# Kernel tuning notes

Measured on AMD Instinct MI355X. Metric: run time of the kernel, lower is better.

Reference implementation:

```python
import jax, jax.numpy as jnp
import numpy as np

VOCAB, E = 50000, 256          # embedding table
WH, SH = 256, 256              # word_hidden_size, sent_hidden_size
DM = WH // 2                   # d_model of both S4Models = 128
NC = (WH // 2) // 2            # complex state modes N//2 = 64
FACTOR = 2
LN_EPS = 1e-5


def _s4model(x, encW, encb, log_dt, Cre, Cim, logAre, Aim, D,
             convW, convb, lng, lnb, d1W, d1b, d2W, d2b, pooling):
    """S4Model forward (eval mode, n_layers=1). x: (B, L, d_input)."""
    x = x @ encW + encb                      # (B, L, H)
    u = jnp.swapaxes(x, -1, -2)              # (B, H, L)
    L = u.shape[-1]
    # --- S4D kernel (Vandermonde) ---
    dt = jnp.exp(log_dt)                     # (H,)
    C = Cre + 1j * Cim                       # (H, N)
    A = -jnp.exp(logAre) + 1j * Aim          # (H, N)
    dtA = A * dt[:, None]                    # (H, N)
    K = jnp.exp(dtA[:, :, None] * jnp.arange(L))           # (H, N, L)
    Ck = C * (jnp.exp(dtA) - 1.0) / A
    k = 2.0 * jnp.einsum('hn,hnl->hl', Ck, K).real         # (H, L)
    # --- FFT convolution ---
    kf = jnp.fft.rfft(k, n=2 * L)            # (H, L+1)
    uf = jnp.fft.rfft(u, n=2 * L)            # (B, H, L+1)
    y = jnp.fft.irfft(uf * kf, n=2 * L)[..., :L]
    y = y + u * D[:, None]
    y = jax.nn.gelu(y, approximate=False)
    # 1x1 conv to 2H then GLU over channel dim
    y = jnp.einsum('oh,bhl->bol', convW, y) + convb[:, None]
    a, b = jnp.split(y, 2, axis=-2)
    z = a * jax.nn.sigmoid(b)
    x = z + u                                # residual
    xt = jnp.swapaxes(x, -1, -2)             # (B, L, H)
    mu = jnp.mean(xt, axis=-1, keepdims=True)
    var = jnp.var(xt, axis=-1, keepdims=True)
    xt = (xt - mu) / jnp.sqrt(var + LN_EPS) * lng + lnb
    h = jax.nn.gelu(xt @ d1W + d1b, approximate=False)
    out = h @ d2W + d2b                      # (B, L, d_output)
    return out.mean(axis=1) if pooling else out


def _model_params(key, d_input, d_model, n, d_output, factor):
    ks = jax.random.split(key, 16)
    H, N = d_model, n
    import math
    p = {}
    p['encW'] = jax.random.normal(ks[0], (d_input, H)) * 0.02
    p['encb'] = jnp.zeros((H,))
    p['log_dt'] = jax.random.uniform(ks[1], (H,)) * (math.log(0.1) - math.log(0.001)) + math.log(0.001)
    p['Cre'] = jax.random.normal(ks[2], (H, N))
    p['Cim'] = jax.random.normal(ks[3], (H, N))
    p['logAre'] = jnp.log(0.5 * jnp.ones((H, N)))
    p['Aim'] = math.pi * jnp.broadcast_to(jnp.arange(N, dtype=jnp.float32), (H, N))
    p['D'] = jax.random.normal(ks[4], (H,))
    p['convW'] = jax.random.normal(ks[5], (2 * H, H)) * 0.05
    p['convb'] = jnp.zeros((2 * H,))
    p['lng'] = jnp.ones((H,))
    p['lnb'] = jnp.zeros((H,))
    p['d1W'] = jax.random.normal(ks[6], (H, H * factor)) * 0.02
    p['d1b'] = jnp.zeros((H * factor,))
    p['d2W'] = jax.random.normal(ks[7], (H * factor, d_output)) * 0.02
    p['d2b'] = jnp.zeros((d_output,))
    return p


def setup_inputs() -> dict:
    key = jax.random.key(0)
    k_ids, k_emb, k_w, k_s = jax.random.split(key, 4)
    inp = {
        'ids': jax.random.randint(k_ids, (8, 64, 512), 0, VOCAB, dtype=jnp.int32),
        'emb': jax.random.normal(k_emb, (VOCAB, E)) * 0.1,
    }
    for pref, k, din, dout in (('w_', k_w, WH, SH), ('s_', k_s, SH, SH)):
        for name, v in _model_params(k, din, DM, NC, dout, FACTOR).items():
            inp[pref + name] = v
    return inp


PNAMES = ['encW', 'encb', 'log_dt', 'Cre', 'Cim', 'logAre', 'Aim', 'D',
          'convW', 'convb', 'lng', 'lnb', 'd1W', 'd1b', 'd2W', 'd2b']


def reference(ids, emb,
              w_encW, w_encb, w_log_dt, w_Cre, w_Cim, w_logAre, w_Aim, w_D,
              w_convW, w_convb, w_lng, w_lnb, w_d1W, w_d1b, w_d2W, w_d2b,
              s_encW, s_encb, s_log_dt, s_Cre, s_Cim, s_logAre, s_Aim, s_D,
              s_convW, s_convb, s_lng, s_lnb, s_d1W, s_d1b, s_d2W, s_d2b):
    B, S, W = ids.shape
    x = emb[ids.reshape(B * S, W)]                       # (B*S, W, E)
    wp = (w_encW, w_encb, w_log_dt, w_Cre, w_Cim, w_logAre, w_Aim, w_D,
          w_convW, w_convb, w_lng, w_lnb, w_d1W, w_d1b, w_d2W, w_d2b)
    sents = _s4model(x, *wp, pooling=True)               # (B*S, SH)
    sents = sents.reshape(B, S, SH)
    sp = (s_encW, s_encb, s_log_dt, s_Cre, s_Cim, s_logAre, s_Aim, s_D,
          s_convW, s_convb, s_lng, s_lnb, s_d1W, s_d1b, s_d2W, s_d2b)
    out = _s4model(sents, *sp, pooling=False)            # (B, S, SH)
    return out  # Euclidean manifold: no clipping / expmap0
```

## Files before the change

kernel.cpp:

```cpp
#include <hip/hip_runtime.h>
#include <hip/hip_bf16.h>

#define DEVINL __device__ __forceinline__

typedef _Float16 f16;
typedef _Float16 f16x8 __attribute__((ext_vector_type(8)));
typedef float f32x4 __attribute__((ext_vector_type(4)));

#define MFMA16 __builtin_amdgcn_mfma_f32_16x16x32_f16

DEVINL float gelu_f(float x) {
    return 0.5f * x * (1.0f + erff(x * 0.70710678118654752440f));
}

__global__ __launch_bounds__(256)
void s4k_kernel(float* __restrict__ kout,
                const float* __restrict__ log_dt,
                const float* __restrict__ Cre,
                const float* __restrict__ Cim,
                const float* __restrict__ logAre,
                const float* __restrict__ Aim,
                int L)
{
    int idx = blockIdx.x * blockDim.x + threadIdx.x;
    int h = idx / L;
    int l = idx - h * L;
    if (h >= 128) return;
    double dt = exp((double)log_dt[h]);
    double acc = 0.0;
    const int N = 64;
    for (int n = 0; n < N; ++n) {
        double Ar = -exp((double)logAre[h * N + n]);
        double Ai = (double)Aim[h * N + n];
        double dr = Ar * dt, di = Ai * dt;
        double edr = exp(dr);
        double sdi = sin(di), cdi = cos(di);
        double Er = edr * cdi - 1.0, Ei = edr * sdi;
        double den = Ar * Ar + Ai * Ai;
        double tr = (Er * Ar + Ei * Ai) / den;
        double ti = (Ei * Ar - Er * Ai) / den;
        double Cr = (double)Cre[h * N + n], Ci = (double)Cim[h * N + n];
        double ckr = Cr * tr - Ci * ti, cki = Cr * ti + Ci * tr;
        double mag = exp(dr * (double)l);
        double ph = di * (double)l;
        acc += ckr * (mag * cos(ph)) - cki * (mag * sin(ph));
    }
    kout[idx] = (float)(2.0 * acc);
}

__global__ __launch_bounds__(256)
void pack_t_kernel(f16* __restrict__ dst, const float* __restrict__ src,
                   int R, int C)
{
    int idx = blockIdx.x * 256 + threadIdx.x;
    int r = idx / C, c = idx - r * C;
    dst[idx] = (f16)src[c * R + r];
}
__global__ __launch_bounds__(256)
void pack_n_kernel(f16* __restrict__ dst, const float* __restrict__ src, int n)
{
    int idx = blockIdx.x * 256 + threadIdx.x;
    if (idx < n) dst[idx] = (f16)src[idx];
}

__global__ __launch_bounds__(256)
void toep_kernel(f16* __restrict__ tf, const float* __restrict__ kW)
{
    int idx = blockIdx.x * 256 + threadIdx.x;
    int r = idx & 7;
    int lane = (idx >> 3) & 63;
    int nn = (idx >> 9) & 3;
    int s = (idx >> 11) & 1;
    int d = (idx >> 12) & 7;
    int h = idx >> 15;
    int widx = 64 * d + 16 * nn + (lane & 15) - 32 * s - 8 * (lane >> 4) - r;
    float v = (widx >= 0 && widx < 512) ? kW[h * 512 + widx] : 0.f;
    tf[idx] = (f16)v;
}

__global__ __launch_bounds__(256)
void enc_mfma(const float* __restrict__ emb, const int* __restrict__ ids,
              long tok_base, const f16* __restrict__ WT ,
              const float* __restrict__ bias, f16* __restrict__ u )
{
    __shared__ f16 As[64][40];
    __shared__ f16 Bs[128][40];
    __shared__ f16 zs[128][72];
    int tid = threadIdx.x;
    int wave = tid >> 6, lane = tid & 63;
    long m0 = (long)blockIdx.x * 64;
    int b_local = (int)(m0 >> 9), l0 = (int)(m0 & 511);

    f32x4 acc[8] = {};

    int am = tid >> 2, aseg = tid & 3;
    int gidx = ids[tok_base + m0 + am];
    const float* aptr = emb + (long)gidx * 256 + aseg * 8;
    int bn = tid >> 1, bseg = tid & 1;
    const f16* bptr = WT + (long)bn * 256 + bseg * 16;

    for (int k0 = 0; k0 < 256; k0 += 32) {
        float4 a0 = *(const float4*)(aptr + k0);
        float4 a1 = *(const float4*)(aptr + k0 + 4);
        f16x8 b0 = *(const f16x8*)(bptr + k0);
        f16x8 b1 = *(const f16x8*)(bptr + k0 + 8);
        __syncthreads();
        f16x8 av;
        av[0]=(f16)a0.x; av[1]=(f16)a0.y; av[2]=(f16)a0.z; av[3]=(f16)a0.w;
        av[4]=(f16)a1.x; av[5]=(f16)a1.y; av[6]=(f16)a1.z; av[7]=(f16)a1.w;
        *(f16x8*)&As[am][aseg * 8] = av;
        *(f16x8*)&Bs[bn][bseg * 16] = b0;
        *(f16x8*)&Bs[bn][bseg * 16 + 8] = b1;
        __syncthreads();
        f16x8 af = *(const f16x8*)&As[16 * wave + (lane & 15)][8 * (lane >> 4)];
#pragma unroll
        for (int nn = 0; nn < 8; ++nn) {
            f16x8 bf = *(const f16x8*)&Bs[nn * 16 + (lane & 15)][8 * (lane >> 4)];
            acc[nn] = MFMA16(af, bf, acc[nn], 0, 0, 0);
        }
    }
    __syncthreads();
#pragma unroll
    for (int nn = 0; nn < 8; ++nn) {
        int h = nn * 16 + (lane & 15);
        float bv = bias[h];
#pragma unroll
        for (int reg = 0; reg < 4; ++reg) {
            int l = 16 * wave + 4 * (lane >> 4) + reg;
            zs[h][l] = (f16)(acc[nn][reg] + bv);
        }
    }
    __syncthreads();
    f16* ub = u + (long)b_local * 65536 + l0;
#pragma unroll
    for (int it = 0; it < 4; ++it) {
        int h = (tid >> 3) + 32 * it, seg = tid & 7;
        *(f16x8*)(ub + (long)h * 512 + seg * 8) = *(const f16x8*)&zs[h][seg * 8];
    }
}

__global__ __launch_bounds__(256)
void conv_mfma(const f16* __restrict__ u, const f16* __restrict__ tf,
               const float* __restrict__ Dv, f16* __restrict__ y, int SC)
{
    __shared__ f16 As[64][72];
    __shared__ f16 ys[64][72];
    int h = blockIdx.x, b0 = blockIdx.y * 64, Lt = blockIdx.z;
    int l0 = Lt * 64;
    int tid = threadIdx.x, wave = tid >> 6, lane = tid & 63;

    f32x4 acc[4] = {};

    int ar = tid >> 2, aseg = tid & 3;
    bool arow_ok = (b0 + ar) < SC;
    const f16* ubase = u + ((long)(b0 + ar) * 128 + h) * 512;

    for (int jt = 0; jt <= Lt; ++jt) {
        f16x8 av0 = {}, av1 = {};
        if (arow_ok) {
            av0 = *(const f16x8*)(ubase + jt * 64 + aseg * 16);
            av1 = *(const f16x8*)(ubase + jt * 64 + aseg * 16 + 8);
        }
        __syncthreads();
        *(f16x8*)&As[ar][aseg * 16]     = av0;
        *(f16x8*)&As[ar][aseg * 16 + 8] = av1;
        __syncthreads();
        int d = Lt - jt;
        const f16* tfb = tf + (((long)h * 8 + d) * 8) * 512 + lane * 8;
#pragma unroll 2
        for (int s = 0; s < 2; ++s) {
            f16x8 af = *(const f16x8*)&As[16 * wave + (lane & 15)][32 * s + 8 * (lane >> 4)];
#pragma unroll
            for (int nn = 0; nn < 4; ++nn) {
                f16x8 bf = *(const f16x8*)(tfb + ((long)s * 4 + nn) * 512);
                acc[nn] = MFMA16(af, bf, acc[nn], 0, 0, 0);
            }
        }
    }
    float Dh = Dv[h];
#pragma unroll
    for (int nn = 0; nn < 4; ++nn) {
#pragma unroll
        for (int reg = 0; reg < 4; ++reg) {
            int bl = 16 * wave + 4 * (lane >> 4) + reg;
            int ll = 16 * nn + (lane & 15);
            float uv = (float)As[bl][ll];
            ys[bl][ll] = (f16)gelu_f(acc[nn][reg] + uv * Dh);
        }
    }
    __syncthreads();
#pragma unroll
    for (int it = 0; it < 2; ++it) {
        int unit = tid + 256 * it;
        int r = unit >> 3, seg = unit & 7;
        if (b0 + r < SC)
            *(f16x8*)(y + ((long)(b0 + r) * 128 + h) * 512 + l0 + seg * 8)
                = *(const f16x8*)&ys[r][seg * 8];
    }
}

__global__ __launch_bounds__(256)
void glu_mfma(const f16* __restrict__ y, const f16* __restrict__ u,
              const f16* __restrict__ WT ,
              const float* __restrict__ cb, const float* __restrict__ lng,
              const float* __restrict__ lnb, f16* __restrict__ xt)
{
    __shared__ f16 At[64][136];
    __shared__ f16 Ut[64][136];
    __shared__ f16 Bs[256][40];
    int b = blockIdx.x, l0 = blockIdx.y * 64;
    int tid = threadIdx.x, wave = tid >> 6, lane = tid & 63;

    f32x4 acc[16] = {};

#pragma unroll
    for (int it = 0; it < 4; ++it) {
        int unit = tid + 256 * it;
        int h = unit >> 3, seg = unit & 7;
        f16x8 v = *(const f16x8*)(y + ((long)b * 128 + h) * 512 + l0 + seg * 8);
        f16x8 w = *(const f16x8*)(u + ((long)b * 128 + h) * 512 + l0 + seg * 8);
#pragma unroll
        for (int q = 0; q < 8; ++q) {
            At[seg * 8 + q][h] = v[q];
            Ut[seg * 8 + q][h] = w[q];
        }
    }
    for (int k0 = 0; k0 < 128; k0 += 32) {
        f16x8 breg[4];
#pragma unroll
        for (int it = 0; it < 4; ++it) {
            int unit = tid + 256 * it;
            int n = unit >> 2, seg = unit & 3;
            breg[it] = *(const f16x8*)(WT + (long)n * 128 + k0 + seg * 8);
        }
        __syncthreads();
#pragma unroll
        for (int it = 0; it < 4; ++it) {
            int unit = tid + 256 * it;
            int n = unit >> 2, seg = unit & 3;
            *(f16x8*)&Bs[n][seg * 8] = breg[it];
        }
        __syncthreads();
        f16x8 af = *(const f16x8*)&At[16 * wave + (lane & 15)][k0 + 8 * (lane >> 4)];
#pragma unroll
        for (int nn = 0; nn < 16; ++nn) {
            f16x8 bf = *(const f16x8*)&Bs[nn * 16 + (lane & 15)][8 * (lane >> 4)];
            acc[nn] = MFMA16(af, bf, acc[nn], 0, 0, 0);
        }
    }
    float zz[8][4];
    float sum[4] = {0.f, 0.f, 0.f, 0.f}, sq[4] = {0.f, 0.f, 0.f, 0.f};
#pragma unroll
    for (int nn = 0; nn < 8; ++nn) {
        int o = nn * 16 + (lane & 15);
        float ca = cb[o], cbb = cb[o + 128];
#pragma unroll
        for (int reg = 0; reg < 4; ++reg) {
            int l = 16 * wave + 4 * (lane >> 4) + reg;
            float a = acc[nn][reg] + ca;
            float bb = acc[nn + 8][reg] + cbb;
            float z = a * (1.0f / (1.0f + expf(-bb))) + (float)Ut[l][o];
            zz[nn][reg] = z;
            sum[reg] += z; sq[reg] += z * z;
        }
    }
#pragma unroll
    for (int d = 1; d < 16; d <<= 1) {
#pragma unroll
        for (int reg = 0; reg < 4; ++reg) {
            sum[reg] += __shfl_xor(sum[reg], d);
            sq[reg] += __shfl_xor(sq[reg], d);
        }
    }
    float mu[4], rs[4];
#pragma unroll
    for (int reg = 0; reg < 4; ++reg) {
        mu[reg] = sum[reg] * (1.0f / 128.0f);
        float var = sq[reg] * (1.0f / 128.0f) - mu[reg] * mu[reg];
        rs[reg] = rsqrtf(var + 1e-5f);
    }
    __syncthreads();
#pragma unroll
    for (int nn = 0; nn < 8; ++nn) {
        int o = nn * 16 + (lane & 15);
        float g = lng[o], bta = lnb[o];
#pragma unroll
        for (int reg = 0; reg < 4; ++reg) {
            int l = 16 * wave + 4 * (lane >> 4) + reg;
            At[l][o] = (f16)((zz[nn][reg] - mu[reg]) * rs[reg] * g + bta);
        }
    }
    __syncthreads();
    f16* xb = xt + ((long)b * 512 + l0) * 128;
#pragma unroll
    for (int it = 0; it < 4; ++it) {
        int unit = tid + 256 * it;
        int l = unit >> 4, seg = unit & 15;
        *(f16x8*)(xb + (long)l * 128 + seg * 8) = *(const f16x8*)&At[l][seg * 8];
    }
}

__global__ __launch_bounds__(256)
void d1_mfma(const f16* __restrict__ xt, const f16* __restrict__ WT ,
             const float* __restrict__ bias, float* __restrict__ hbar,
             long tok_base)
{
    __shared__ f16 At[64][136];
    __shared__ f16 Bs[256][40];
    __shared__ float red[4][16][16];
    int tid = threadIdx.x, wave = tid >> 6, lane = tid & 63;
    long m0 = (long)blockIdx.x * 64;

    f32x4 acc[16] = {};

#pragma unroll
    for (int it = 0; it < 4; ++it) {
        int unit = tid + 256 * it;
        int r = unit >> 4, seg = unit & 15;
        *(f16x8*)&At[r][seg * 8] = *(const f16x8*)(xt + (m0 + r) * 128 + seg * 8);
    }
    for (int k0 = 0; k0 < 128; k0 += 32) {
        f16x8 breg[4];
#pragma unroll
        for (int it = 0; it < 4; ++it) {
            int unit = tid + 256 * it;
            int n = unit >> 2, seg = unit & 3;
            breg[it] = *(const f16x8*)(WT + (long)n * 128 + k0 + seg * 8);
        }
        __syncthreads();
#pragma unroll
        for (int it = 0; it < 4; ++it) {
            int unit = tid + 256 * it;
            int n = unit >> 2, seg = unit & 3;
            *(f16x8*)&Bs[n][seg * 8] = breg[it];
        }
        __syncthreads();
        f16x8 af = *(const f16x8*)&At[16 * wave + (lane & 15)][k0 + 8 * (lane >> 4)];
#pragma unroll
        for (int nn = 0; nn < 16; ++nn) {
            f16x8 bf = *(const f16x8*)&Bs[nn * 16 + (lane & 15)][8 * (lane >> 4)];
            acc[nn] = MFMA16(af, bf, acc[nn], 0, 0, 0);
        }
    }
    long sent = (tok_base + m0) >> 9;
#pragma unroll
    for (int nn = 0; nn < 16; ++nn) {
        int o = nn * 16 + (lane & 15);
        float bv = bias[o];
        float s = 0.f;
#pragma unroll
        for (int reg = 0; reg < 4; ++reg)
            s += gelu_f(acc[nn][reg] + bv);
        s += __shfl_xor(s, 16);
        s += __shfl_xor(s, 32);
        if (lane < 16) red[wave][lane][nn] = s;
    }
    __syncthreads();
    if (wave == 0 && lane < 16) {
#pragma unroll
        for (int nn = 0; nn < 16; ++nn) {
            float tot = red[0][lane][nn] + red[1][lane][nn]
                      + red[2][lane][nn] + red[3][lane][nn];
            atomicAdd(&hbar[sent * 256 + nn * 16 + lane], tot * (1.0f / 512.0f));
        }
    }
}

__global__ __launch_bounds__(256)
void gemm_kernel(const float* __restrict__ A, const int* __restrict__ gather,
                 const float* __restrict__ W, const float* __restrict__ bias,
                 float* __restrict__ C, float* __restrict__ pool,
                 long m_base, int K, int N, int act, int poolLen)
{
    __shared__ float As[32][68];
    __shared__ float Ws[32][128];
    __shared__ float red[16][128];

    int tid = threadIdx.x;
    int tx = tid & 15, ty = tid >> 4;
    long m0 = (long)blockIdx.x * 64;
    int n0 = blockIdx.y * 128;

    int la_row = tid >> 2, la_k = (tid & 3) * 8;
    long arow = gather ? (long)gather[m_base + m0 + la_row] : (m0 + la_row);
    const float* Arow = A + arow * (long)K + la_k;
    int wk = tid >> 3, wn = (tid & 7) * 16;
    const float* Wp = W + (long)wk * N + n0 + wn;

    float acc[4][8];
#pragma unroll
    for (int i = 0; i < 4; ++i)
#pragma unroll
        for (int j = 0; j < 8; ++j) acc[i][j] = 0.f;

    for (int k0 = 0; k0 < K; k0 += 32) {
        float4 a0 = *(const float4*)(Arow + k0);
        float4 a1 = *(const float4*)(Arow + k0 + 4);
        const float* wp = Wp + (long)k0 * N;
        float4 w0 = *(const float4*)(wp);
        float4 w1 = *(const float4*)(wp + 4);
        float4 w2 = *(const float4*)(wp + 8);
        float4 w3 = *(const float4*)(wp + 12);
        __syncthreads();
        As[la_k + 0][la_row] = a0.x; As[la_k + 1][la_row] = a0.y;
        As[la_k + 2][la_row] = a0.z; As[la_k + 3][la_row] = a0.w;
        As[la_k + 4][la_row] = a1.x; As[la_k + 5][la_row] = a1.y;
        As[la_k + 6][la_row] = a1.z; As[la_k + 7][la_row] = a1.w;
        *(float4*)&Ws[wk][wn]      = w0;
        *(float4*)&Ws[wk][wn + 4]  = w1;
        *(float4*)&Ws[wk][wn + 8]  = w2;
        *(float4*)&Ws[wk][wn + 12] = w3;
        __syncthreads();
#pragma unroll
        for (int kk = 0; kk < 32; ++kk) {
            float4 av  = *(const float4*)&As[kk][ty * 4];
            float4 wv0 = *(const float4*)&Ws[kk][tx * 4];
            float4 wv1 = *(const float4*)&Ws[kk][64 + tx * 4];
            float a_[4] = {av.x, av.y, av.z, av.w};
            float w_[8] = {wv0.x, wv0.y, wv0.z, wv0.w, wv1.x, wv1.y, wv1.z, wv1.w};
#pragma unroll
            for (int i = 0; i < 4; ++i)
#pragma unroll
                for (int j = 0; j < 8; ++j)
                    acc[i][j] = fmaf(a_[i], w_[j], acc[i][j]);
        }
    }

    float bv[8];
#pragma unroll
    for (int j = 0; j < 8; ++j) {
        int col = (j < 4) ? (tx * 4 + j) : (64 + tx * 4 + (j - 4));
        bv[j] = bias[n0 + col];
    }
#pragma unroll
    for (int i = 0; i < 4; ++i)
#pragma unroll
        for (int j = 0; j < 8; ++j) {
            float v = acc[i][j] + bv[j];
            if (act == 1) v = gelu_f(v);
            acc[i][j] = v;
        }

    if (pool) {
        float pv[8];
#pragma unroll
        for (int j = 0; j < 8; ++j)
            pv[j] = acc[0][j] + acc[1][j] + acc[2][j] + acc[3][j];
        __syncthreads();
#pragma unroll
        for (int j = 0; j < 8; ++j) {
            int col = (j < 4) ? (tx * 4 + j) : (64 + tx * 4 + (j - 4));
            red[ty][col] = pv[j];
        }
        __syncthreads();
        if (ty == 0) {
            long sent = (m_base + m0) / poolLen;
            float inv = 1.0f / (float)poolLen;
#pragma unroll
            for (int j = 0; j < 8; ++j) {
                int col = (j < 4) ? (tx * 4 + j) : (64 + tx * 4 + (j - 4));
                float s = 0.f;
#pragma unroll
                for (int t = 0; t < 16; ++t) s += red[t][col];
                atomicAdd(&pool[sent * N + n0 + col], s * inv);
            }
        }
    } else if (C) {
#pragma unroll
        for (int i = 0; i < 4; ++i) {
            long m = m0 + ty * 4 + i;
            float* cp = C + m * (long)N + n0;
            float4 s0 = {acc[i][0], acc[i][1], acc[i][2], acc[i][3]};
            float4 s1 = {acc[i][4], acc[i][5], acc[i][6], acc[i][7]};
            *(float4*)(cp + tx * 4) = s0;
            *(float4*)(cp + 64 + tx * 4) = s1;
        }
    }
}

__global__ __launch_bounds__(256)
void transpose_kernel(const float* __restrict__ in, float* __restrict__ out,
                      int L, int H)
{
    __shared__ float t[32][33];
    int b = blockIdx.x, l0 = blockIdx.y * 32, h0 = blockIdx.z * 32;
    int tid = threadIdx.x;
    int c = tid & 31, r = tid >> 5;
    const float* ib = in + ((long)b * L + l0) * H + h0;
#pragma unroll
    for (int i = 0; i < 4; ++i)
        t[r + 8 * i][c] = ib[(long)(r + 8 * i) * H + c];
    __syncthreads();
    float* ob = out + ((long)b * H + h0) * L + l0;
#pragma unroll
    for (int i = 0; i < 4; ++i)
        ob[(long)(r + 8 * i) * L + c] = t[c][r + 8 * i];
}

__global__ __launch_bounds__(256)
void conv_kernel(const float* __restrict__ u, const float* __restrict__ kmat,
                 float* __restrict__ y, int NB, int L)
{
    __shared__ float Ut[64][68];
    __shared__ float kwin[128];
    int h = blockIdx.x;
    int b0 = blockIdx.y * 64, l0 = blockIdx.z * 64;
    int tid = threadIdx.x, tx = tid & 15, ty = tid >> 4;
    const float* kh = kmat + (long)h * L;

    float acc[4][4];
#pragma unroll
    for (int i = 0; i < 4; ++i)
#pragma unroll
        for (int j = 0; j < 4; ++j) acc[i][j] = 0.f;

    int ur = tid >> 2, uc = (tid & 3) * 16;

    for (int j0 = 0; j0 <= l0 + 63; j0 += 64) {
        float4 u0 = {0,0,0,0}, u1 = {0,0,0,0}, u2 = {0,0,0,0}, u3 = {0,0,0,0};
        if (b0 + ur < NB) {
            const float* up = u + ((long)(b0 + ur) * 128 + h) * L + j0 + uc;
            u0 = *(const float4*)up;        u1 = *(const float4*)(up + 4);
            u2 = *(const float4*)(up + 8);  u3 = *(const float4*)(up + 12);
        }
        float kv_ = 0.f;
        int d = l0 - j0 - 63 + tid;
        if (tid < 128) kv_ = (d >= 0 && d < L) ? kh[d] : 0.f;
        __syncthreads();
        {
            float uv[16] = {u0.x,u0.y,u0.z,u0.w, u1.x,u1.y,u1.z,u1.w,
                            u2.x,u2.y,u2.z,u2.w, u3.x,u3.y,u3.z,u3.w};
#pragma unroll
            for (int q = 0; q < 16; ++q) Ut[uc + q][ur] = uv[q];
        }
        if (tid < 128) kwin[tid] = kv_;
        __syncthreads();
#pragma unroll
        for (int jj = 0; jj < 64; ++jj) {
            float4 uv = *(const float4*)&Ut[jj][ty * 4];
            float ub[4] = {uv.x, uv.y, uv.z, uv.w};
            float kj[4];
#pragma unroll
            for (int j = 0; j < 4; ++j) kj[j] = kwin[63 + tx * 4 + j - jj];
#pragma unroll
            for (int i = 0; i < 4; ++i)
#pragma unroll
                for (int j = 0; j < 4; ++j)
                    acc[i][j] = fmaf(ub[i], kj[j], acc[i][j]);
        }
    }
#pragma unroll
    for (int i = 0; i < 4; ++i) {
        int b = b0 + ty * 4 + i;
        if (b < NB) {
            float4 s = {acc[i][0], acc[i][1], acc[i][2], acc[i][3]};
            *(float4*)(y + ((long)b * 128 + h) * L + l0 + tx * 4) = s;
        }
    }
}

__global__ __launch_bounds__(256)
void skipgelu_kernel(float* __restrict__ y, const float* __restrict__ u,
                     const float* __restrict__ D, int log2L, long total)
{
    long i = (long)blockIdx.x * 256 + threadIdx.x;
    long stride = (long)gridDim.x * 256;
    for (; i < total; i += stride) {
        int h = (int)((i >> log2L) & 127);
        float v = y[i] + u[i] * D[h];
        y[i] = gelu_f(v);
    }
}

__global__ __launch_bounds__(256)
void glu_kernel(const float* __restrict__ convW, const float* __restrict__ convb,
                const float* __restrict__ g, const float* u,
                float* z, int L)
{
    __shared__ float Wa[32][68], Wb[32][68], Gs[32][72];
    int b = blockIdx.x, o0 = blockIdx.y * 64, l0 = blockIdx.z * 64;
    int tid = threadIdx.x, tx = tid & 15, ty = tid >> 4;
    const float* gb = g + (long)b * 128 * L;

    float aa[4][4], ab[4][4];
#pragma unroll
    for (int i = 0; i < 4; ++i)
#pragma unroll
        for (int j = 0; j < 4; ++j) { aa[i][j] = 0.f; ab[i][j] = 0.f; }

    int wr = tid >> 2, wc = (tid & 3) * 8;
    int gh = tid >> 3, gl = (tid & 7) * 8;

    for (int k0 = 0; k0 < 128; k0 += 32) {
        float4 wa0 = *(const float4*)(convW + (long)(o0 + wr) * 128 + k0 + wc);
        float4 wa1 = *(const float4*)(convW + (long)(o0 + wr) * 128 + k0 + wc + 4);
        float4 wb0 = *(const float4*)(convW + (long)(o0 + wr + 128) * 128 + k0 + wc);
        float4 wb1 = *(const float4*)(convW + (long)(o0 + wr + 128) * 128 + k0 + wc + 4);
        float4 g0 = *(const float4*)(gb + (long)(k0 + gh) * L + l0 + gl);
        float4 g1 = *(const float4*)(gb + (long)(k0 + gh) * L + l0 + gl + 4);
        __syncthreads();
        {
            float wav[8] = {wa0.x,wa0.y,wa0.z,wa0.w, wa1.x,wa1.y,wa1.z,wa1.w};
            float wbv[8] = {wb0.x,wb0.y,wb0.z,wb0.w, wb1.x,wb1.y,wb1.z,wb1.w};
#pragma unroll
            for (int q = 0; q < 8; ++q) { Wa[wc + q][wr] = wav[q]; Wb[wc + q][wr] = wbv[q]; }
        }
        *(float4*)&Gs[gh][gl]     = g0;
        *(float4*)&Gs[gh][gl + 4] = g1;
        __syncthreads();
#pragma unroll
        for (int kk = 0; kk < 32; ++kk) {
            float4 wav = *(const float4*)&Wa[kk][ty * 4];
            float4 wbv = *(const float4*)&Wb[kk][ty * 4];
            float4 gv  = *(const float4*)&Gs[kk][tx * 4];
            float wa_[4] = {wav.x, wav.y, wav.z, wav.w};
            float wb_[4] = {wbv.x, wbv.y, wbv.z, wbv.w};
            float g_[4]  = {gv.x, gv.y, gv.z, gv.w};
#pragma unroll
            for (int i = 0; i < 4; ++i)
#pragma unroll
                for (int j = 0; j < 4; ++j) {
                    aa[i][j] = fmaf(wa_[i], g_[j], aa[i][j]);
                    ab[i][j] = fmaf(wb_[i], g_[j], ab[i][j]);
                }
        }
    }
#pragma unroll
    for (int i = 0; i < 4; ++i) {
        int o = o0 + ty * 4 + i;
        float ca = convb[o], cb2 = convb[o + 128];
        const float* up = u + ((long)b * 128 + o) * L + l0 + tx * 4;
        float4 uv = *(const float4*)up;
        float uu[4] = {uv.x, uv.y, uv.z, uv.w};
        float tmp[4];
#pragma unroll
        for (int j = 0; j < 4; ++j) {
            float av = aa[i][j] + ca;
            float bv2 = ab[i][j] + cb2;
            tmp[j] = av * (1.0f / (1.0f + expf(-bv2))) + uu[j];
        }
        float4 outv = {tmp[0], tmp[1], tmp[2], tmp[3]};
        *(float4*)(z + ((long)b * 128 + o) * L + l0 + tx * 4) = outv;
    }
}

__global__ __launch_bounds__(256)
void ln_kernel(const float* __restrict__ z, const float* __restrict__ gamma,
               const float* __restrict__ beta, float* __restrict__ out, int L)
{
    __shared__ float zs[128][65];
    __shared__ float mu_s[64], rs_s[64];
    int b = blockIdx.x, l0 = blockIdx.y * 64;
    const float* zb = z + (long)b * 128 * L;
    int tid = threadIdx.x;
    for (int idx = tid; idx < 128 * 64; idx += 256) {
        int h = idx >> 6, li = idx & 63;
        zs[h][li] = zb[(long)h * L + l0 + li];
    }
    __syncthreads();
    int l = tid >> 2, sub = tid & 3;
    float s = 0.f, sq = 0.f;
    for (int ii = 0; ii < 32; ++ii) {
        int i = (ii + sub * 8) & 31;
        float v = zs[sub * 32 + i][l];
        s += v; sq += v * v;
    }
    s += __shfl_xor(s, 1); sq += __shfl_xor(sq, 1);
    s += __shfl_xor(s, 2); sq += __shfl_xor(sq, 2);
    if (sub == 0) {
        float mu = s * (1.0f / 128.0f);
        float var = sq * (1.0f / 128.0f) - mu * mu;
        mu_s[l] = mu;
        rs_s[l] = rsqrtf(var + 1e-5f);
    }
    __syncthreads();
    for (int idx = tid; idx < 64 * 128; idx += 256) {
        int li = idx >> 7, h = idx & 127;
        float v = (zs[h][li] - mu_s[li]) * rs_s[li];
        out[((long)b * L + l0 + li) * 128 + h] = v * gamma[h] + beta[h];
    }
}

extern "C" void kernel_launch(void* const* d_in, const int* in_sizes, int n_in,
                              void* d_out, int out_size, void* d_ws, size_t ws_size,
                              hipStream_t stream)
{
    const int* ids = (const int*)d_in[0];
    const float* emb = (const float*)d_in[1];
    const float* const* wp = (const float* const*)(d_in + 2);
    const float* const* sp = (const float* const*)(d_in + 18);
    enum {ENCW = 0, ENCB, LOGDT, CRE, CIM, LOGARE, AIM, DD,
          CONVW, CONVB, LNG, LNB, D1W, D1B, D2W, D2B};

    char* p = (char*)d_ws;
    auto alloc = [&](size_t bytes) {
        char* r = p; p += (bytes + 255) & ~(size_t)255; return r;
    };
    float* kW    = (float*)alloc(128 * 512 * 4);
    float* kS    = (float*)alloc(128 * 64 * 4);
    float* sents = (float*)alloc(512 * 256 * 4);
    float* hbar  = (float*)alloc(512 * 256 * 4);
    float* su    = (float*)alloc(512 * 128 * 4);
    float* subhl = (float*)alloc(512 * 128 * 4);
    float* sy    = (float*)alloc(512 * 128 * 4);
    float* szb   = (float*)alloc(512 * 128 * 4);
    float* sxt   = (float*)alloc(512 * 128 * 4);
    float* sh    = (float*)alloc(512 * 256 * 4);
    f16* encWT   = (f16*)alloc(128 * 256 * 2);
    f16* convWT  = (f16*)alloc(256 * 128 * 2);
    f16* d1WT    = (f16*)alloc(256 * 128 * 2);
    f16* tf      = (f16*)alloc(4194304 * 2);

    long avail = (long)ws_size - (long)(p - (char*)d_ws);
    int SC = 512;
    while (SC > 1 && 3L * SC * 65536 * 2 + 1024 > avail) SC >>= 1;
    int nch = 512 / SC;
    f16* u_c  = (f16*)alloc((size_t)SC * 65536 * 2);
    f16* y_c  = (f16*)alloc((size_t)SC * 65536 * 2);
    f16* xt_c = (f16*)alloc((size_t)SC * 65536 * 2);

    hipMemsetAsync(hbar, 0, 512 * 256 * 4, stream);
    s4k_kernel<<<256, 256, 0, stream>>>(
        kW, wp[LOGDT], wp[CRE], wp[CIM], wp[LOGARE], wp[AIM], 512);
    s4k_kernel<<<32, 256, 0, stream>>>(
        kS, sp[LOGDT], sp[CRE], sp[CIM], sp[LOGARE], sp[AIM], 64);
    pack_t_kernel<<<128, 256, 0, stream>>>(encWT, wp[ENCW], 128, 256);
    pack_n_kernel<<<128, 256, 0, stream>>>(convWT, wp[CONVW], 32768);
    pack_t_kernel<<<128, 256, 0, stream>>>(d1WT, wp[D1W], 256, 128);
    toep_kernel<<<16384, 256, 0, stream>>>(tf, kW);

    for (int c = 0; c < nch; ++c) {
        long tok_base = (long)c * SC * 512;
        enc_mfma<<<SC * 8, 256, 0, stream>>>(
            emb, ids, tok_base, encWT, wp[ENCB], u_c);
        conv_mfma<<<dim3(128, (SC + 63) / 64, 8), 256, 0, stream>>>(
            u_c, tf, wp[DD], y_c, SC);
        glu_mfma<<<dim3(SC, 8), 256, 0, stream>>>(
            y_c, u_c, convWT, wp[CONVB], wp[LNG], wp[LNB], xt_c);
        d1_mfma<<<SC * 8, 256, 0, stream>>>(
            xt_c, d1WT, wp[D1B], hbar, tok_base);
    }
    gemm_kernel<<<dim3(8, 2), 256, 0, stream>>>(
        hbar, nullptr, wp[D2W], wp[D2B], sents, nullptr, 0, 256, 256, 0, 0);

    gemm_kernel<<<dim3(8, 1), 256, 0, stream>>>(
        sents, nullptr, sp[ENCW], sp[ENCB], su, nullptr, 0, 256, 128, 0, 0);
    transpose_kernel<<<dim3(8, 2, 4), 256, 0, stream>>>(su, subhl, 64, 128);
    conv_kernel<<<dim3(128, 1, 1), 256, 0, stream>>>(subhl, kS, sy, 8, 64);
    skipgelu_kernel<<<256, 256, 0, stream>>>(sy, subhl, sp[DD], 6, 8L * 128 * 64);
    glu_kernel<<<dim3(8, 2, 1), 256, 0, stream>>>(
        sp[CONVW], sp[CONVB], sy, subhl, szb, 64);
    ln_kernel<<<dim3(8, 1), 256, 0, stream>>>(szb, sp[LNG], sp[LNB], sxt, 64);
    gemm_kernel<<<dim3(8, 2), 256, 0, stream>>>(
        sxt, nullptr, sp[D1W], sp[D1B], sh, nullptr, 0, 128, 256, 1, 0);
    gemm_kernel<<<dim3(8, 2), 256, 0, stream>>>(
        sh, nullptr, sp[D2W], sp[D2B], (float*)d_out, nullptr, 0, 256, 256, 0, 0);
}
```

Baseline: 676.9 us.

## Fuse GLU/LN with dense1, restructure conv loop, precompute fp16 embeddings, faster S4 kernel

Several changes at once. The S4D kernel generator now builds powers of exp(dtA) in shared memory, split into a 32x16 decomposition, instead of calling exp/sin/cos per (l,n). The embedding table is converted to fp16 once. The causal Toeplitz conv now runs one block over all 8 L-tiles and reuses each u tile across output tiles. The GLU+LayerNorm kernel is fused with the dense1+GELU+mean kernel using an XOR-swizzled LDS layout, which removes the xt round trip through global memory. In exchange, the fp16 embedding conversion writes the full 50000x256 table on every call. The conv also holds 32 accumulators per thread, which raises register pressure and lowers grid parallelism to 128x8 blocks.

```diff
diff --git a/kernel.cpp b/kernel.cpp
--- a/kernel.cpp
+++ b/kernel.cpp
@@ -4,6 +4,7 @@
 #define DEVINL __device__ __forceinline__
 
 typedef _Float16 f16;
+typedef _Float16 f16x2 __attribute__((ext_vector_type(2)));
 typedef _Float16 f16x8 __attribute__((ext_vector_type(8)));
 typedef float f32x4 __attribute__((ext_vector_type(4)));
 
@@ -13,39 +14,59 @@
     return 0.5f * x * (1.0f + erff(x * 0.70710678118654752440f));
 }
 
-__global__ __launch_bounds__(256)
-void s4k_kernel(float* __restrict__ kout,
-                const float* __restrict__ log_dt,
-                const float* __restrict__ Cre,
-                const float* __restrict__ Cim,
-                const float* __restrict__ logAre,
-                const float* __restrict__ Aim,
-                int L)
-{
-    int idx = blockIdx.x * blockDim.x + threadIdx.x;
-    int h = idx / L;
-    int l = idx - h * L;
-    if (h >= 128) return;
-    double dt = exp((double)log_dt[h]);
-    double acc = 0.0;
-    const int N = 64;
-    for (int n = 0; n < N; ++n) {
-        double Ar = -exp((double)logAre[h * N + n]);
-        double Ai = (double)Aim[h * N + n];
+DEVINL int swz(int col, int row) {
+    return (((col >> 3) ^ (row & 7)) << 3) | (col & 7);
+}
+
+__global__ __launch_bounds__(256)
+void s4k2_kernel(float* __restrict__ kout,
+                 const float* __restrict__ log_dt, const float* __restrict__ Cre,
+                 const float* __restrict__ Cim, const float* __restrict__ logAre,
+                 const float* __restrict__ Aim, int L)
+{
+    __shared__ double EaR[64][16], EaI[64][16];
+    __shared__ double EbR[64][32], EbI[64][32];
+    __shared__ double CkR[64], CkI[64];
+    int h = blockIdx.x, tid = threadIdx.x;
+    if (tid < 64) {
+        int n = tid;
+        double dt = exp((double)log_dt[h]);
+        double Ar = -exp((double)logAre[h * 64 + n]);
+        double Ai = (double)Aim[h * 64 + n];
         double dr = Ar * dt, di = Ai * dt;
         double edr = exp(dr);
-        double sdi = sin(di), cdi = cos(di);
-        double Er = edr * cdi - 1.0, Ei = edr * sdi;
+        double E1r = edr * cos(di), E1i = edr * sin(di);
         double den = Ar * Ar + Ai * Ai;
-        double tr = (Er * Ar + Ei * Ai) / den;
-        double ti = (Ei * Ar - Er * Ai) / den;
-        double Cr = (double)Cre[h * N + n], Ci = (double)Cim[h * N + n];
-        double ckr = Cr * tr - Ci * ti, cki = Cr * ti + Ci * tr;
-        double mag = exp(dr * (double)l);
-        double ph = di * (double)l;
-        acc += ckr * (mag * cos(ph)) - cki * (mag * sin(ph));
-    }
-    kout[idx] = (float)(2.0 * acc);
+        double tr = ((E1r - 1.0) * Ar + E1i * Ai) / den;
+        double ti = (E1i * Ar - (E1r - 1.0) * Ai) / den;
+        double Cr = (double)Cre[h * 64 + n], Ci = (double)Cim[h * 64 + n];
+        CkR[n] = Cr * tr - Ci * ti;
+        CkI[n] = Cr * ti + Ci * tr;
+        double br = 1.0, bi = 0.0;
+        for (int b2 = 0; b2 < 32; ++b2) {
+            EbR[n][b2] = br; EbI[n][b2] = bi;
+            double nr = br * E1r - bi * E1i;
+            bi = br * E1i + bi * E1r; br = nr;
+        }
+        double E32r = br, E32i = bi;
+        double ar2 = 1.0, ai2 = 0.0;
+        for (int a = 0; a < 16; ++a) {
+            EaR[n][a] = ar2; EaI[n][a] = ai2;
+            double nr = ar2 * E32r - ai2 * E32i;
+            ai2 = ar2 * E32i + ai2 * E32r; ar2 = nr;
+        }
+    }
+    __syncthreads();
+    for (int l = tid; l < L; l += 256) {
+        int a = l >> 5, b2 = l & 31;
+        double acc = 0.0;
+        for (int n = 0; n < 64; ++n) {
+            double er = EaR[n][a] * EbR[n][b2] - EaI[n][a] * EbI[n][b2];
+            double ei = EaR[n][a] * EbI[n][b2] + EaI[n][a] * EbR[n][b2];
+            acc += CkR[n] * er - CkI[n] * ei;
+        }
+        kout[h * L + l] = (float)(2.0 * acc);
+    }
 }
 
 __global__ __launch_bounds__(256)
@@ -61,6 +82,17 @@
 {
     int idx = blockIdx.x * 256 + threadIdx.x;
     if (idx < n) dst[idx] = (f16)src[idx];
+}
+__global__ __launch_bounds__(256)
+void packemb_kernel(f16* __restrict__ dst, const float* __restrict__ src)
+{
+    long i = ((long)blockIdx.x * 256 + threadIdx.x) * 8;
+    float4 a = *(const float4*)(src + i);
+    float4 b = *(const float4*)(src + i + 4);
+    f16x8 o;
+    o[0]=(f16)a.x; o[1]=(f16)a.y; o[2]=(f16)a.z; o[3]=(f16)a.w;
+    o[4]=(f16)b.x; o[5]=(f16)b.y; o[6]=(f16)b.z; o[7]=(f16)b.w;
+    *(f16x8*)(dst + i) = o;
 }
 
 __global__ __launch_bounds__(256)
@@ -79,9 +111,9 @@
 }
 
 __global__ __launch_bounds__(256)
-void enc_mfma(const float* __restrict__ emb, const int* __restrict__ ids,
+void enc_mfma(const f16* __restrict__ emb16, const int* __restrict__ ids,
               long tok_base, const f16* __restrict__ WT ,
-              const float* __restrict__ bias, f16* __restrict__ u )
+              const float* __restrict__ bias, f16* __restrict__ u)
 {
     __shared__ f16 As[64][40];
     __shared__ f16 Bs[128][40];
@@ -95,19 +127,15 @@
 
     int am = tid >> 2, aseg = tid & 3;
     int gidx = ids[tok_base + m0 + am];
-    const float* aptr = emb + (long)gidx * 256 + aseg * 8;
+    const f16* aptr = emb16 + (long)gidx * 256 + aseg * 8;
     int bn = tid >> 1, bseg = tid & 1;
     const f16* bptr = WT + (long)bn * 256 + bseg * 16;
 
     for (int k0 = 0; k0 < 256; k0 += 32) {
-        float4 a0 = *(const float4*)(aptr + k0);
-        float4 a1 = *(const float4*)(aptr + k0 + 4);
+        f16x8 av = *(const f16x8*)(aptr + k0);
         f16x8 b0 = *(const f16x8*)(bptr + k0);
         f16x8 b1 = *(const f16x8*)(bptr + k0 + 8);
         __syncthreads();
-        f16x8 av;
-        av[0]=(f16)a0.x; av[1]=(f16)a0.y; av[2]=(f16)a0.z; av[3]=(f16)a0.w;
-        av[4]=(f16)a1.x; av[5]=(f16)a1.y; av[6]=(f16)a1.z; av[7]=(f16)a1.w;
         *(f16x8*)&As[am][aseg * 8] = av;
         *(f16x8*)&Bs[bn][bseg * 16] = b0;
         *(f16x8*)&Bs[bn][bseg * 16 + 8] = b1;
@@ -140,22 +168,22 @@
 }
 
 __global__ __launch_bounds__(256)
-void conv_mfma(const f16* __restrict__ u, const f16* __restrict__ tf,
-               const float* __restrict__ Dv, f16* __restrict__ y, int SC)
+void conv2_mfma(const f16* __restrict__ u, const f16* __restrict__ tf,
+                const float* __restrict__ Dv, f16* __restrict__ y, int SC)
 {
     __shared__ f16 As[64][72];
     __shared__ f16 ys[64][72];
-    int h = blockIdx.x, b0 = blockIdx.y * 64, Lt = blockIdx.z;
-    int l0 = Lt * 64;
+    int h = blockIdx.x, b0 = blockIdx.y * 64;
     int tid = threadIdx.x, wave = tid >> 6, lane = tid & 63;
-
-    f32x4 acc[4] = {};
-
+    float Dh = Dv[h];
     int ar = tid >> 2, aseg = tid & 3;
     bool arow_ok = (b0 + ar) < SC;
     const f16* ubase = u + ((long)(b0 + ar) * 128 + h) * 512;
 
-    for (int jt = 0; jt <= Lt; ++jt) {
+    f32x4 acc[8][4] = {};
+
+#pragma unroll
+    for (int jt = 0; jt < 8; ++jt) {
         f16x8 av0 = {}, av1 = {};
         if (arow_ok) {
             av0 = *(const f16x8*)(ubase + jt * 64 + aseg * 16);
@@ -165,66 +193,80 @@
         *(f16x8*)&As[ar][aseg * 16]     = av0;
         *(f16x8*)&As[ar][aseg * 16 + 8] = av1;
         __syncthreads();
-        int d = Lt - jt;
-        const f16* tfb = tf + (((long)h * 8 + d) * 8) * 512 + lane * 8;
-#pragma unroll 2
-        for (int s = 0; s < 2; ++s) {
-            f16x8 af = *(const f16x8*)&As[16 * wave + (lane & 15)][32 * s + 8 * (lane >> 4)];
-#pragma unroll
-            for (int nn = 0; nn < 4; ++nn) {
-                f16x8 bf = *(const f16x8*)(tfb + ((long)s * 4 + nn) * 512);
-                acc[nn] = MFMA16(af, bf, acc[nn], 0, 0, 0);
+#pragma unroll
+        for (int Lt = jt; Lt < 8; ++Lt) {
+            const f16* tfb = tf + (((long)h * 8 + (Lt - jt)) * 8) * 512 + lane * 8;
+#pragma unroll
+            for (int s = 0; s < 2; ++s) {
+                f16x8 af = *(const f16x8*)&As[16 * wave + (lane & 15)][32 * s + 8 * (lane >> 4)];
+#pragma unroll
+                for (int nn = 0; nn < 4; ++nn) {
+                    f16x8 bf = *(const f16x8*)(tfb + ((long)s * 4 + nn) * 512);
+                    acc[Lt][nn] = MFMA16(af, bf, acc[Lt][nn], 0, 0, 0);
+                }
             }
         }
-    }
-    float Dh = Dv[h];
-#pragma unroll
-    for (int nn = 0; nn < 4; ++nn) {
-#pragma unroll
-        for (int reg = 0; reg < 4; ++reg) {
-            int bl = 16 * wave + 4 * (lane >> 4) + reg;
-            int ll = 16 * nn + (lane & 15);
-            float uv = (float)As[bl][ll];
-            ys[bl][ll] = (f16)gelu_f(acc[nn][reg] + uv * Dh);
-        }
-    }
-    __syncthreads();
+#pragma unroll
+        for (int nn = 0; nn < 4; ++nn) {
+#pragma unroll
+            for (int reg = 0; reg < 4; ++reg) {
+                int bl = 16 * wave + 4 * (lane >> 4) + reg;
+                int ll = 16 * nn + (lane & 15);
+                ys[bl][ll] = (f16)gelu_f(acc[jt][nn][reg] + (float)As[bl][ll] * Dh);
+            }
+        }
+        __syncthreads();
+#pragma unroll
+        for (int it = 0; it < 2; ++it) {
+            int unit = tid + 256 * it;
+            int r = unit >> 3, seg = unit & 7;
+            if (b0 + r < SC)
+                *(f16x8*)(y + ((long)(b0 + r) * 128 + h) * 512 + jt * 64 + seg * 8)
+                    = *(const f16x8*)&ys[r][seg * 8];
+        }
+    }
+}
+
+#define PITCH 144
+__global__ __launch_bounds__(256)
+void gld_mfma(const f16* __restrict__ y, const f16* __restrict__ u,
+              const f16* __restrict__ WT ,
+              const float* __restrict__ cb, const float* __restrict__ lng,
+              const float* __restrict__ lnb,
+              const f16* __restrict__ W1T ,
+              const float* __restrict__ b1, float* __restrict__ hbar,
+              long sent_base)
+{
+    __shared__ f16 At[64][PITCH];
+    __shared__ f16 Ut[64][PITCH];
+    __shared__ f16 Bs[256][40];
+    __shared__ float red[4][16][16];
+    int b = blockIdx.x, l0 = blockIdx.y * 64;
+    int tid = threadIdx.x, wave = tid >> 6, lane = tid & 63;
+
 #pragma unroll
     for (int it = 0; it < 2; ++it) {
         int unit = tid + 256 * it;
-        int r = unit >> 3, seg = unit & 7;
-        if (b0 + r < SC)
-            *(f16x8*)(y + ((long)(b0 + r) * 128 + h) * 512 + l0 + seg * 8)
-                = *(const f16x8*)&ys[r][seg * 8];
-    }
-}
-
-__global__ __launch_bounds__(256)
-void glu_mfma(const f16* __restrict__ y, const f16* __restrict__ u,
-              const f16* __restrict__ WT ,
-              const float* __restrict__ cb, const float* __restrict__ lng,
-              const float* __restrict__ lnb, f16* __restrict__ xt)
-{
-    __shared__ f16 At[64][136];
-    __shared__ f16 Ut[64][136];
-    __shared__ f16 Bs[256][40];
-    int b = blockIdx.x, l0 = blockIdx.y * 64;
-    int tid = threadIdx.x, wave = tid >> 6, lane = tid & 63;
+        int hp = unit & 63, seg = unit >> 6;
+        int h = hp * 2;
+        const f16* yp = y + ((long)b * 128 + h) * 512 + l0 + seg * 8;
+        const f16* up = u + ((long)b * 128 + h) * 512 + l0 + seg * 8;
+        f16x8 ya = *(const f16x8*)yp;
+        f16x8 yb = *(const f16x8*)(yp + 512);
+        f16x8 ua = *(const f16x8*)up;
+        f16x8 ub = *(const f16x8*)(up + 512);
+#pragma unroll
+        for (int q = 0; q < 8; ++q) {
+            int l = seg * 8 + q;
+            int ix = swz(h, l);
+            f16x2 py; py[0] = ya[q]; py[1] = yb[q];
+            f16x2 pu; pu[0] = ua[q]; pu[1] = ub[q];
+            *(f16x2*)&At[l][ix] = py;
+            *(f16x2*)&Ut[l][ix] = pu;
+        }
+    }
 
     f32x4 acc[16] = {};
-
-#pragma unroll
-    for (int it = 0; it < 4; ++it) {
-        int unit = tid + 256 * it;
-        int h = unit >> 3, seg = unit & 7;
-        f16x8 v = *(const f16x8*)(y + ((long)b * 128 + h) * 512 + l0 + seg * 8);
-        f16x8 w = *(const f16x8*)(u + ((long)b * 128 + h) * 512 + l0 + seg * 8);
-#pragma unroll
-        for (int q = 0; q < 8; ++q) {
-            At[seg * 8 + q][h] = v[q];
-            Ut[seg * 8 + q][h] = w[q];
-        }
-    }
     for (int k0 = 0; k0 < 128; k0 += 32) {
         f16x8 breg[4];
 #pragma unroll
@@ -241,15 +283,17 @@
             *(f16x8*)&Bs[n][seg * 8] = breg[it];
         }
         __syncthreads();
-        f16x8 af = *(const f16x8*)&At[16 * wave + (lane & 15)][k0 + 8 * (lane >> 4)];
+        int arow = 16 * wave + (lane & 15);
+        f16x8 af = *(const f16x8*)&At[arow][swz(k0 + 8 * (lane >> 4), arow)];
 #pragma unroll
         for (int nn = 0; nn < 16; ++nn) {
             f16x8 bf = *(const f16x8*)&Bs[nn * 16 + (lane & 15)][8 * (lane >> 4)];
             acc[nn] = MFMA16(af, bf, acc[nn], 0, 0, 0);
         }
     }
+
     float zz[8][4];
-    float sum[4] = {0.f, 0.f, 0.f, 0.f}, sq[4] = {0.f, 0.f, 0.f, 0.f};
+    float sum[4] = {0.f,0.f,0.f,0.f}, sq[4] = {0.f,0.f,0.f,0.f};
 #pragma unroll
     for (int nn = 0; nn < 8; ++nn) {
         int o = nn * 16 + (lane & 15);
@@ -258,8 +302,8 @@
         for (int reg = 0; reg < 4; ++reg) {
             int l = 16 * wave + 4 * (lane >> 4) + reg;
             float a = acc[nn][reg] + ca;
-            float bb = acc[nn + 8][reg] + cbb;
-            float z = a * (1.0f / (1.0f + expf(-bb))) + (float)Ut[l][o];
+            float bbv = acc[nn + 8][reg] + cbb;
+            float z = a * (1.0f / (1.0f + expf(-bbv))) + (float)Ut[l][swz(o, l)];
             zz[nn][reg] = z;
             sum[reg] += z; sq[reg] += z * z;
         }
@@ -269,7 +313,7 @@
 #pragma unroll
         for (int reg = 0; reg < 4; ++reg) {
             sum[reg] += __shfl_xor(sum[reg], d);
-            sq[reg] += __shfl_xor(sq[reg], d);
+            sq[reg]  += __shfl_xor(sq[reg], d);
         }
     }
     float mu[4], rs[4];
@@ -287,45 +331,18 @@
 #pragma unroll
         for (int reg = 0; reg < 4; ++reg) {
             int l = 16 * wave + 4 * (lane >> 4) + reg;
-            At[l][o] = (f16)((zz[nn][reg] - mu[reg]) * rs[reg] * g + bta);
-        }
-    }
-    __syncthreads();
-    f16* xb = xt + ((long)b * 512 + l0) * 128;
-#pragma unroll
-    for (int it = 0; it < 4; ++it) {
-        int unit = tid + 256 * it;
-        int l = unit >> 4, seg = unit & 15;
-        *(f16x8*)(xb + (long)l * 128 + seg * 8) = *(const f16x8*)&At[l][seg * 8];
-    }
-}
-
-__global__ __launch_bounds__(256)
-void d1_mfma(const f16* __restrict__ xt, const f16* __restrict__ WT ,
-             const float* __restrict__ bias, float* __restrict__ hbar,
-             long tok_base)
-{
-    __shared__ f16 At[64][136];
-    __shared__ f16 Bs[256][40];
-    __shared__ float red[4][16][16];
-    int tid = threadIdx.x, wave = tid >> 6, lane = tid & 63;
-    long m0 = (long)blockIdx.x * 64;
-
-    f32x4 acc[16] = {};
-
-#pragma unroll
-    for (int it = 0; it < 4; ++it) {
-        int unit = tid + 256 * it;
-        int r = unit >> 4, seg = unit & 15;
-        *(f16x8*)&At[r][seg * 8] = *(const f16x8*)(xt + (m0 + r) * 128 + seg * 8);
-    }
+            At[l][swz(o, l)] = (f16)((zz[nn][reg] - mu[reg]) * rs[reg] * g + bta);
+        }
+    }
+
+    f32x4 acc2[16] = {};
     for (int k0 = 0; k0 < 128; k0 += 32) {
         f16x8 breg[4];
 #pragma unroll
         for (int it = 0; it < 4; ++it) {
             int unit = tid + 256 * it;
             int n = unit >> 2, seg = unit & 3;
-            breg[it] = *(const f16x8*)(WT + (long)n * 128 + k0 + seg * 8);
+            breg[it] = *(const f16x8*)(W1T + (long)n * 128 + k0 + seg * 8);
         }
         __syncthreads();
 #pragma unroll
@@ -335,22 +352,23 @@
             *(f16x8*)&Bs[n][seg * 8] = breg[it];
         }
         __syncthreads();
-        f16x8 af = *(const f16x8*)&At[16 * wave + (lane & 15)][k0 + 8 * (lane >> 4)];
+        int arow = 16 * wave + (lane & 15);
+        f16x8 af = *(const f16x8*)&At[arow][swz(k0 + 8 * (lane >> 4), arow)];
 #pragma unroll
         for (int nn = 0; nn < 16; ++nn) {
             f16x8 bf = *(const f16x8*)&Bs[nn * 16 + (lane & 15)][8 * (lane >> 4)];
-            acc[nn] = MFMA16(af, bf, acc[nn], 0, 0, 0);
-        }
-    }
-    long sent = (tok_base + m0) >> 9;
+            acc2[nn] = MFMA16(af, bf, acc2[nn], 0, 0, 0);
+        }
+    }
+
+    long sent = sent_base + b;
 #pragma unroll
     for (int nn = 0; nn < 16; ++nn) {
-        int o = nn * 16 + (lane & 15);
-        float bv = bias[o];
+        float bv = b1[nn * 16 + (lane & 15)];
         float s = 0.f;
 #pragma unroll
         for (int reg = 0; reg < 4; ++reg)
-            s += gelu_f(acc[nn][reg] + bv);
+            s += gelu_f(acc2[nn][reg] + bv);
         s += __shfl_xor(s, 16);
         s += __shfl_xor(s, 32);
         if (lane < 16) red[wave][lane][nn] = s;
@@ -709,20 +727,21 @@
     f16* encWT   = (f16*)alloc(128 * 256 * 2);
     f16* convWT  = (f16*)alloc(256 * 128 * 2);
     f16* d1WT    = (f16*)alloc(256 * 128 * 2);
-    f16* tf      = (f16*)alloc(4194304 * 2);
+    f16* tf      = (f16*)alloc(4194304L * 2);
+    f16* emb16   = (f16*)alloc(12800000L * 2);
 
     long avail = (long)ws_size - (long)(p - (char*)d_ws);
     int SC = 512;
-    while (SC > 1 && 3L * SC * 65536 * 2 + 1024 > avail) SC >>= 1;
+    while (SC > 1 && 2L * SC * 131072 + 1024 > avail) SC >>= 1;
     int nch = 512 / SC;
-    f16* u_c  = (f16*)alloc((size_t)SC * 65536 * 2);
-    f16* y_c  = (f16*)alloc((size_t)SC * 65536 * 2);
-    f16* xt_c = (f16*)alloc((size_t)SC * 65536 * 2);
+    f16* u_c = (f16*)alloc((size_t)SC * 65536 * 2);
+    f16* y_c = (f16*)alloc((size_t)SC * 65536 * 2);
 
     hipMemsetAsync(hbar, 0, 512 * 256 * 4, stream);
-    s4k_kernel<<<256, 256, 0, stream>>>(
+    packemb_kernel<<<6250, 256, 0, stream>>>(emb16, emb);
+    s4k2_kernel<<<128, 256, 0, stream>>>(
         kW, wp[LOGDT], wp[CRE], wp[CIM], wp[LOGARE], wp[AIM], 512);
-    s4k_kernel<<<32, 256, 0, stream>>>(
+    s4k2_kernel<<<128, 256, 0, stream>>>(
         kS, sp[LOGDT], sp[CRE], sp[CIM], sp[LOGARE], sp[AIM], 64);
     pack_t_kernel<<<128, 256, 0, stream>>>(encWT, wp[ENCW], 128, 256);
     pack_n_kernel<<<128, 256, 0, stream>>>(convWT, wp[CONVW], 32768);
@@ -732,13 +751,12 @@
     for (int c = 0; c < nch; ++c) {
         long tok_base = (long)c * SC * 512;
         enc_mfma<<<SC * 8, 256, 0, stream>>>(
-            emb, ids, tok_base, encWT, wp[ENCB], u_c);
-        conv_mfma<<<dim3(128, (SC + 63) / 64, 8), 256, 0, stream>>>(
+            emb16, ids, tok_base, encWT, wp[ENCB], u_c);
+        conv2_mfma<<<dim3(128, (SC + 63) / 64), 256, 0, stream>>>(
             u_c, tf, wp[DD], y_c, SC);
-        glu_mfma<<<dim3(SC, 8), 256, 0, stream>>>(
-            y_c, u_c, convWT, wp[CONVB], wp[LNG], wp[LNB], xt_c);
-        d1_mfma<<<SC * 8, 256, 0, stream>>>(
-            xt_c, d1WT, wp[D1B], hbar, tok_base);
+        gld_mfma<<<dim3(SC, 8), 256, 0, stream>>>(
+            y_c, u_c, convWT, wp[CONVB], wp[LNG], wp[LNB],
+            d1WT, wp[D1B], hbar, (long)c * SC);
     }
     gemm_kernel<<<dim3(8, 2), 256, 0, stream>>>(
         hbar, nullptr, wp[D2W], wp[D2B], sents, nullptr, 0, 256, 256, 0, 0);
```

New measurement: 786.5 us. +16.2%, slower.
